# Performance work log

Measured on AMD Instinct MI355X. Metric: run time of the kernel, lower is better.

The kernel has to match this reference:

```python
import jax, jax.numpy as jnp
import numpy as np

B, N, K, H, NHEADS, NIN = 4, 2000, 30, 128, 4, 256
DFF = 4 * H
EPS = 1e-6


def layer_norm(x, gain, bias):
    # torch .var() defaults to unbiased (ddof=1); denominator is (sigma + eps)
    mu = x.mean(-1, keepdims=True)
    sigma = jnp.sqrt(x.var(-1, ddof=1, keepdims=True) + EPS)
    return gain * (x - mu) / (sigma + EPS) + bias


def setup_inputs() -> dict:
    key = jax.random.key(0)
    ks = jax.random.split(key, 10)
    s = 0.05
    h_v = jax.random.normal(ks[0], (B, N, H), jnp.float32)
    h_e = jax.random.normal(ks[1], (B, N, K, NIN), jnp.float32)
    mask_attend = (jax.random.uniform(ks[2], (B, N, K)) < 0.9).astype(jnp.float32)
    mask_attend = mask_attend.at[..., 0].set(1.0)  # avoid all-masked rows -> NaN softmax
    mask_v = (jax.random.uniform(ks[3], (B, N)) < 0.95).astype(jnp.float32)
    return {
        "h_v": h_v,
        "h_e": h_e,
        "mask_v": mask_v,
        "mask_attend": mask_attend,
        "W_Q": jax.random.normal(ks[4], (H, H), jnp.float32) * s,
        "W_K": jax.random.normal(ks[5], (H, NIN), jnp.float32) * s,
        "W_V": jax.random.normal(ks[6], (H, NIN), jnp.float32) * s,
        "W_O": jax.random.normal(ks[7], (H, H), jnp.float32) * s,
        "gain0": jnp.ones((H,), jnp.float32),
        "bias0": jnp.zeros((H,), jnp.float32),
        "gain1": jnp.ones((H,), jnp.float32),
        "bias1": jnp.zeros((H,), jnp.float32),
        "W_in": jax.random.normal(ks[8], (DFF, H), jnp.float32) * s,
        "b_in": jnp.zeros((DFF,), jnp.float32),
        "W_out": jax.random.normal(ks[9], (H, DFF), jnp.float32) * s,
        "b_out": jnp.zeros((H,), jnp.float32),
    }


def reference(h_v, h_e, mask_v, mask_attend, W_Q, W_K, W_V, W_O,
              gain0, bias0, gain1, bias1, W_in, b_in, W_out, b_out):
    d = H // NHEADS
    # Neighbor attention (dropout is identity at inference)
    Q = (h_v @ W_Q.T).reshape(B, N, NHEADS, d)          # [B,N,h,d]
    Kp = (h_e @ W_K.T).reshape(B, N, K, NHEADS, d)      # [B,N,K,h,d]
    Vp = (h_e @ W_V.T).reshape(B, N, K, NHEADS, d)      # [B,N,K,h,d]
    logits = jnp.einsum('bnhd,bnkhd->bnhk', Q, Kp) / np.sqrt(d)
    mask = mask_attend[:, :, None, :]                   # [B,N,1,K] broadcast over heads
    neg_inf = jnp.finfo(logits.dtype).min
    attend = jax.nn.softmax(jnp.where(mask > 0, logits, neg_inf), axis=-1) * mask
    h_upd = jnp.einsum('bnhk,bnkhd->bnhd', attend, Vp).reshape(B, N, H)
    dh = h_upd @ W_O.T
    h = layer_norm(h_v + dh, gain0, bias0)
    # Position-wise FFN
    dh = jax.nn.relu(h @ W_in.T + b_in) @ W_out.T + b_out
    h = layer_norm(h + dh, gain1, bias1)
    return mask_v[..., None] * h
```

## Files before the change

kernel.cpp:

```cpp
#include <hip/hip_runtime.h>
#include <math.h>

#define TK 30
#define TH 128
#define TNIN 256
#define TDFF 512
#define NTOK 8000
#define ROWP 264

typedef __attribute__((ext_vector_type(8))) short short8v;
typedef __attribute__((ext_vector_type(4))) short short4v;
typedef __attribute__((ext_vector_type(4))) float f32x4;

constexpr float LN_EPS = 1e-6f;
constexpr float NEG_INF = -3.402823466e38f;
constexpr float INV_SQRT_D = 0.17677669529663687f;

static __device__ __forceinline__ unsigned short f2bf(float f) {
  unsigned u = __float_as_uint(f);
  u = u + 0x7fffu + ((u >> 16) & 1u);
  return (unsigned short)(u >> 16);
}
static __device__ __forceinline__ float bf2f(unsigned short s) {
  return __uint_as_float(((unsigned)s) << 16);
}
static __device__ __forceinline__ void gload16(const void* gsrc, void* ldst) {
  __builtin_amdgcn_global_load_lds(
      (const __attribute__((address_space(1))) unsigned int*)gsrc,
      (__attribute__((address_space(3))) unsigned int*)ldst, 16, 0, 0);
}

__global__ void conv_weights_kernel(const float* __restrict__ W_K,
                                    const float* __restrict__ W_V,
                                    const float* __restrict__ W_Q,
                                    const float* __restrict__ W_in,
                                    const float* __restrict__ W_out,
                                    unsigned short* __restrict__ Wc2,
                                    unsigned short* __restrict__ Wq2,
                                    unsigned short* __restrict__ Wi2,
                                    unsigned short* __restrict__ Wo2)
{
  int idx = blockIdx.x * 256 + threadIdx.x;
  if (idx < 65536) {
    int e = idx >> 3, j = idx & 7;
    int kk = e >> 10, n = (e >> 6) & 15, lane = e & 63;
    int r = n*16 + (lane & 15);
    int c = kk*32 + (lane >> 4)*8 + j;
    float v = (r < TH) ? W_K[(size_t)r*TNIN + c] : W_V[(size_t)(r-TH)*TNIN + c];
    Wc2[idx] = f2bf(v);
  } else if (idx < 81920) {
    int i2 = idx - 65536;
    int e = i2 >> 3, j = i2 & 7;
    int kk = e >> 9, n = (e >> 6) & 7, lane = e & 63;
    int r = n*16 + (lane & 15);
    int c = kk*32 + (lane >> 4)*8 + j;
    Wq2[i2] = f2bf(W_Q[(size_t)r*TH + c]);
  } else if (idx < 147456) {
    int i3 = idx - 81920;
    int e = i3 >> 3, j = i3 & 7;
    int ks = e >> 11, n = (e >> 6) & 31, lane = e & 63;
    int r = n*16 + (lane & 15);
    int c = ks*32 + (lane >> 4)*8 + j;
    Wi2[i3] = f2bf(W_in[(size_t)r*TH + c]);
  } else {
    int i4 = idx - 147456;
    int e = i4 >> 3, j = i4 & 7;
    int ks = e >> 9, n = (e >> 6) & 7, lane = e & 63;
    int r = n*16 + (lane & 15);
    int c = ks*32 + (lane >> 4)*8 + j;
    Wo2[i4] = f2bf(W_out[(size_t)r*TDFF + c]);
  }
}

__global__ __launch_bounds__(512, 4) void kvattn_kernel(
    const float* __restrict__ A, const unsigned short* __restrict__ Wc2,
    const unsigned short* __restrict__ Qg, const float* __restrict__ mask_attend,
    float* __restrict__ ul)
{
  const int tid  = threadIdx.x;
  const int wave = tid >> 6;
  const int lane = tid & 63;
  const int lm   = lane & 15;
  const int lgp  = lane >> 4;
  const int mh   = wave >> 2;
  const int nq   = wave & 3;

  __shared__ __align__(16) char smem[69632];
  unsigned short* Bl  = (unsigned short*)smem;
  unsigned short* Al  = (unsigned short*)(smem + 49152);
  unsigned short* KVs = (unsigned short*)smem;
  float* att = (float*)(smem + 67584);

  const int rowa = tid >> 2, cga = tid & 3;
  const int rowc = (rowa > 119) ? 119 : rowa;
  const float* aptr = A + ((size_t)blockIdx.x*120 + rowc)*TNIN + cga*8;

  #define ISSUE_B(K)                                                             \
    { gload16(Wc2 + (size_t)(K)*8192 + tid*8,       &Bl[((K)%3)*8192 + tid*8]);  \
      gload16(Wc2 + (size_t)(K)*8192 + (tid+512)*8, &Bl[((K)%3)*8192 + (tid+512)*8]); }

  #define WRITE_A(K, S)                                                     \
    { short8v w;                                                            \
      w[0]=(short)f2bf(ra[S][0].x); w[1]=(short)f2bf(ra[S][0].y);           \
      w[2]=(short)f2bf(ra[S][0].z); w[3]=(short)f2bf(ra[S][0].w);           \
      w[4]=(short)f2bf(ra[S][1].x); w[5]=(short)f2bf(ra[S][1].y);           \
      w[6]=(short)f2bf(ra[S][1].z); w[7]=(short)f2bf(ra[S][1].w);           \
      *(short8v*)&Al[(((K)&1)*128 + rowa)*40 + cga*8] = w; }

  float4 ra[3][2];
  f32x4 acc[4][4] = {};

  ra[0][0] = *(const float4*)(aptr + 0);
  ra[0][1] = *(const float4*)(aptr + 4);
  ISSUE_B(0);
  ISSUE_B(1);
  ra[1][0] = *(const float4*)(aptr + 32);
  ra[1][1] = *(const float4*)(aptr + 36);
  ra[2][0] = *(const float4*)(aptr + 64);
  ra[2][1] = *(const float4*)(aptr + 68);
  WRITE_A(0, 0);

  #pragma unroll
  for (int k = 0; k < 8; ++k) {
    if (k == 7)      asm volatile("s_waitcnt vmcnt(0)" ::: "memory");
    else if (k == 6) asm volatile("s_waitcnt vmcnt(4)" ::: "memory");
    else             asm volatile("s_waitcnt vmcnt(6)" ::: "memory");
    __builtin_amdgcn_s_barrier();

    if (k < 6) ISSUE_B(k+2);
    if (k < 5) {
      ra[k%3][0] = *(const float4*)(aptr + (k+3)*32);
      ra[k%3][1] = *(const float4*)(aptr + (k+3)*32 + 4);
    }

    short8v af[4];
    #pragma unroll
    for (int m = 0; m < 4; ++m)
      af[m] = *(const short8v*)&Al[((k&1)*128 + mh*64 + m*16 + lm)*40 + lgp*8];

    #pragma unroll
    for (int n = 0; n < 4; ++n) {
      short8v b = *(const short8v*)&Bl[(k%3)*8192 + ((nq*4 + n)*64 + lane)*8];
      #pragma unroll
      for (int m = 0; m < 4; ++m)
        acc[m][n] = __builtin_amdgcn_mfma_f32_16x16x32_bf16(b, af[m], acc[m][n], 0, 0, 0);
    }

    if (k < 7) WRITE_A(k+1, (k+1)%3);
  }
  #undef ISSUE_B
  #undef WRITE_A

  __syncthreads();

  #pragma unroll
  for (int m = 0; m < 4; ++m) {
    int row = mh*64 + m*16 + lm;
    #pragma unroll
    for (int n = 0; n < 4; ++n) {
      int col = nq*64 + n*16 + lgp*4;
      short4v p;
      p[0]=(short)f2bf(acc[m][n][0]); p[1]=(short)f2bf(acc[m][n][1]);
      p[2]=(short)f2bf(acc[m][n][2]); p[3]=(short)f2bf(acc[m][n][3]);
      *(short4v*)&KVs[row*ROWP + col] = p;
    }
  }
  __syncthreads();

  {
    int tok = tid >> 7, h = (tid >> 5) & 3, k = tid & 31;
    int gtok = blockIdx.x*4 + tok;
    float s = 0.f;
    float ma = 0.f;
    if (k < TK) {
      const unsigned short* qp = Qg + (size_t)gtok*TH + h*32;
      const unsigned short* kp = &KVs[(tok*TK + k)*ROWP + h*32];
      #pragma unroll
      for (int j = 0; j < 4; ++j) {
        short8v qf = *(const short8v*)(qp + j*8);
        short8v kf = *(const short8v*)(kp + j*8);
        #pragma unroll
        for (int e = 0; e < 8; ++e)
          s += bf2f((unsigned short)qf[e]) * bf2f((unsigned short)kf[e]);
      }
      ma = mask_attend[(size_t)gtok*TK + k];
    }
    bool ok = (k < TK) && (ma > 0.f);
    float val = ok ? s * INV_SQRT_D : NEG_INF;
    float mm = val;
    #pragma unroll
    for (int d = 16; d >= 1; d >>= 1) mm = fmaxf(mm, __shfl_xor(mm, d, 32));
    float e = ok ? expf(val - mm) : 0.f;
    float ss = e;
    #pragma unroll
    for (int d = 16; d >= 1; d >>= 1) ss += __shfl_xor(ss, d, 32);
    att[(tok*4 + h)*32 + k] = e / ss;
  }
  __syncthreads();

  {
    int tok = tid >> 7, c = tid & 127;
    int gtok = blockIdx.x*4 + tok;
    const float* ar = &att[(tok*4 + (c >> 5))*32];
    const unsigned short* vb = &KVs[tok*TK*ROWP + TH + c];
    float u = 0.f;
    #pragma unroll
    for (int k = 0; k < TK; ++k)
      u += ar[k] * bf2f(vb[k*ROWP]);
    ul[(size_t)gtok*TH + c] = u;
  }
}

__global__ __launch_bounds__(512, 4) void q_gemm_kernel(
    const float* __restrict__ h_v, const unsigned short* __restrict__ Wq2,
    unsigned short* __restrict__ Qg)
{
  const int m0   = blockIdx.x * 128;
  const int tid  = threadIdx.x;
  const int wave = tid >> 6;
  const int lane = tid & 63;
  const int lm   = lane & 15;
  const int lgp  = lane >> 4;
  const int mh   = wave >> 2;
  const int nq   = wave & 3;

  __shared__ __align__(16) char smem[53248];
  unsigned short* Bq = (unsigned short*)smem;
  unsigned short* Al = (unsigned short*)(smem + 32768);
  unsigned short* Ct = (unsigned short*)smem;

  const int rowa = tid >> 2, cga = tid & 3;
  int rc = m0 + rowa; if (rc > NTOK-1) rc = NTOK-1;
  const float* aptr = h_v + (size_t)rc*TH + cga*8;

  #define WRITE_A(K, S)                                                     \
    { short8v w;                                                            \
      w[0]=(short)f2bf(ra[S][0].x); w[1]=(short)f2bf(ra[S][0].y);           \
      w[2]=(short)f2bf(ra[S][0].z); w[3]=(short)f2bf(ra[S][0].w);           \
      w[4]=(short)f2bf(ra[S][1].x); w[5]=(short)f2bf(ra[S][1].y);           \
      w[6]=(short)f2bf(ra[S][1].z); w[7]=(short)f2bf(ra[S][1].w);           \
      *(short8v*)&Al[(((K)&1)*128 + rowa)*40 + cga*8] = w; }

  float4 ra[2][2];
  f32x4 acc[4][2] = {};

  ra[0][0] = *(const float4*)(aptr + 0);
  ra[0][1] = *(const float4*)(aptr + 4);
  #pragma unroll
  for (int p = 0; p < 4; ++p)
    gload16(Wq2 + (size_t)(tid + p*512)*8, &Bq[(tid + p*512)*8]);
  ra[1][0] = *(const float4*)(aptr + 32);
  ra[1][1] = *(const float4*)(aptr + 36);
  WRITE_A(0, 0);

  #pragma unroll
  for (int k = 0; k < 4; ++k) {
    if (k == 0) asm volatile("s_waitcnt vmcnt(2)" ::: "memory");
    __builtin_amdgcn_s_barrier();

    if (k < 2) {
      ra[k&1][0] = *(const float4*)(aptr + (k+2)*32);
      ra[k&1][1] = *(const float4*)(aptr + (k+2)*32 + 4);
    }

    short8v af[4];
    #pragma unroll
    for (int m = 0; m < 4; ++m)
      af[m] = *(const short8v*)&Al[((k&1)*128 + mh*64 + m*16 + lm)*40 + lgp*8];

    #pragma unroll
    for (int n = 0; n < 2; ++n) {
      short8v b = *(const short8v*)&Bq[((k*8 + nq*2 + n)*64 + lane)*8];
      #pragma unroll
      for (int m = 0; m < 4; ++m)
        acc[m][n] = __builtin_amdgcn_mfma_f32_16x16x32_bf16(b, af[m], acc[m][n], 0, 0, 0);
    }

    if (k < 3) WRITE_A(k+1, (k+1)&1);
  }
  #undef WRITE_A

  __syncthreads();
  #pragma unroll
  for (int m = 0; m < 4; ++m) {
    int row = mh*64 + m*16 + lm;
    #pragma unroll
    for (int n = 0; n < 2; ++n) {
      int col = nq*32 + n*16 + lgp*4;
      short4v p;
      p[0]=(short)f2bf(acc[m][n][0]); p[1]=(short)f2bf(acc[m][n][1]);
      p[2]=(short)f2bf(acc[m][n][2]); p[3]=(short)f2bf(acc[m][n][3]);
      *(short4v*)&Ct[row*136 + col] = p;
    }
  }
  __syncthreads();
  #pragma unroll
  for (int p = 0; p < 4; ++p) {
    int t = p*512 + tid;
    int row = t >> 4, cg = t & 15;
    if (m0 + row < NTOK)
      *(short8v*)&Qg[(size_t)(m0 + row)*TH + cg*8] =
          *(const short8v*)&Ct[row*136 + cg*8];
  }
}

__global__ __launch_bounds__(256) void wo_ln_kernel(
    const float* __restrict__ ul, const float* __restrict__ W_O,
    const float* __restrict__ h_v, const float* __restrict__ gain0,
    const float* __restrict__ bias0, float* __restrict__ Hn)
{
  const int tid  = threadIdx.x;
  const int tok0 = blockIdx.x * 32;
  __shared__ float Aa[32][128];
  __shared__ float Wt[128][128];

  for (int t = tid; t < 32*32; t += 256) {
    int row = t >> 5, i4 = t & 31;
    *(float4*)&Aa[row][i4*4] = *(const float4*)&ul[(size_t)(tok0+row)*TH + i4*4];
  }
  for (int t = tid; t < 128*32; t += 256) {
    int f = t & 127, i4 = t >> 7;
    float4 w = *(const float4*)&W_O[(size_t)f*TH + i4*4];
    Wt[i4*4+0][f]=w.x; Wt[i4*4+1][f]=w.y; Wt[i4*4+2][f]=w.z; Wt[i4*4+3][f]=w.w;
  }
  __syncthreads();

  const int tokg = tid>>5, colg = tid&31;
  float acc[4][4] = {};
  for (int i = 0; i < TH; i += 4){
    float a[4][4];
    #pragma unroll
    for (int r=0;r<4;r++){
      float4 tv=*(const float4*)&Aa[tokg*4+r][i];
      a[r][0]=tv.x;a[r][1]=tv.y;a[r][2]=tv.z;a[r][3]=tv.w;
    }
    #pragma unroll
    for (int d=0; d<4; ++d){
      float4 wv = *(const float4*)&Wt[i+d][colg*4];
      #pragma unroll
      for (int r=0;r<4;r++){
        acc[r][0]+=a[r][d]*wv.x; acc[r][1]+=a[r][d]*wv.y;
        acc[r][2]+=a[r][d]*wv.z; acc[r][3]+=a[r][d]*wv.w;
      }
    }
  }

  float4 g  = *(const float4*)&gain0[colg*4];
  float4 bb = *(const float4*)&bias0[colg*4];
  #pragma unroll
  for (int r=0;r<4;r++){
    int tok = tok0 + tokg*4 + r;
    float4 hv = *(const float4*)&h_v[(size_t)tok*TH + colg*4];
    float x0 = acc[r][0]+hv.x;
    float x1 = acc[r][1]+hv.y;
    float x2 = acc[r][2]+hv.z;
    float x3 = acc[r][3]+hv.w;
    float s1 = x0+x1+x2+x3;
    float s2 = x0*x0+x1*x1+x2*x2+x3*x3;
    #pragma unroll
    for (int m=16;m>=1;m>>=1){ s1 += __shfl_xor(s1,m,32); s2 += __shfl_xor(s2,m,32); }
    float mu  = s1*(1.f/128.f);
    float var = (s2 - 128.f*mu*mu)*(1.f/127.f);
    float inv = 1.f/(sqrtf(var+LN_EPS)+LN_EPS);
    float4 y;
    y.x = g.x*(x0-mu)*inv + bb.x;
    y.y = g.y*(x1-mu)*inv + bb.y;
    y.z = g.z*(x2-mu)*inv + bb.z;
    y.w = g.w*(x3-mu)*inv + bb.w;
    *(float4*)&Hn[(size_t)tok*TH + colg*4] = y;
  }
}

__global__ __launch_bounds__(256) void ffn_fused_kernel(
    const float* __restrict__ Hn, const unsigned short* __restrict__ Wi2,
    const unsigned short* __restrict__ Wo2,
    const float* __restrict__ b_in, const float* __restrict__ b_out,
    const float* __restrict__ gain1, const float* __restrict__ bias1,
    const float* __restrict__ mask_v, float* __restrict__ out)
{
  const int tid  = threadIdx.x;
  const int tok0 = blockIdx.x * 32;
  const int wave = tid >> 6;
  const int lane = tid & 63;
  const int lm   = lane & 15;
  const int lgp  = lane >> 4;

  __shared__ __align__(16) char bst_mem[32768];
  __shared__ __align__(16) unsigned short At[32][136];
  __shared__ __align__(16) unsigned short Zs[32][520];
  __shared__ float bin[512];
  unsigned short* Bst = (unsigned short*)bst_mem;
  float* Xs = (float*)bst_mem;

  for (int t = tid; t < 1024; t += 256) {
    int row = t >> 5, q = t & 31;
    float4 v = *(const float4*)&Hn[(size_t)(tok0+row)*TH + q*4];
    short4v w;
    w[0]=(short)f2bf(v.x); w[1]=(short)f2bf(v.y);
    w[2]=(short)f2bf(v.z); w[3]=(short)f2bf(v.w);
    *(short4v*)&At[row][q*4] = w;
  }
  if (tid < 128) *(float4*)&bin[tid*4] = *(const float4*)&b_in[tid*4];

  f32x4 acc1[2][8] = {};
  #pragma unroll
  for (int ks = 0; ks < 4; ++ks) {
    #pragma unroll
    for (int p = 0; p < 8; ++p)
      gload16(Wi2 + (size_t)ks*16384 + (tid + p*256)*8, &Bst[(tid + p*256)*8]);
    asm volatile("s_waitcnt vmcnt(0)" ::: "memory");
    __syncthreads();

    short8v a0 = *(const short8v*)&At[lm]     [ks*32 + lgp*8];
    short8v a1 = *(const short8v*)&At[16 + lm][ks*32 + lgp*8];
    #pragma unroll
    for (int n = 0; n < 8; ++n) {
      short8v b = *(const short8v*)&Bst[((wave*8 + n)*64 + lane)*8];
      acc1[0][n] = __builtin_amdgcn_mfma_f32_16x16x32_bf16(b, a0, acc1[0][n], 0, 0, 0);
      acc1[1][n] = __builtin_amdgcn_mfma_f32_16x16x32_bf16(b, a1, acc1[1][n], 0, 0, 0);
    }
    __syncthreads();
  }

  #pragma unroll
  for (int m = 0; m < 2; ++m) {
    int row = m*16 + lm;
    #pragma unroll
    for (int n = 0; n < 8; ++n) {
      int col = (wave*8 + n)*16 + lgp*4;
      float4 bv = *(const float4*)&bin[col];
      short4v p;
      p[0]=(short)f2bf(fmaxf(acc1[m][n][0] + bv.x, 0.f));
      p[1]=(short)f2bf(fmaxf(acc1[m][n][1] + bv.y, 0.f));
      p[2]=(short)f2bf(fmaxf(acc1[m][n][2] + bv.z, 0.f));
      p[3]=(short)f2bf(fmaxf(acc1[m][n][3] + bv.w, 0.f));
      *(short4v*)&Zs[row][col] = p;
    }
  }
  __syncthreads();

  f32x4 acc2[2][2] = {};
  #pragma unroll
  for (int ks2 = 0; ks2 < 8; ++ks2) {
    #pragma unroll
    for (int p = 0; p < 4; ++p)
      gload16(Wo2 + (size_t)ks2*8192 + (tid + p*256)*8, &Bst[(tid + p*256)*8]);
    asm volatile("s_waitcnt vmcnt(0)" ::: "memory");
    __syncthreads();

    #pragma unroll
    for (int s = 0; s < 2; ++s) {
      int ks = ks2*2 + s;
      short8v a0 = *(const short8v*)&Zs[lm]     [ks*32 + lgp*8];
      short8v a1 = *(const short8v*)&Zs[16 + lm][ks*32 + lgp*8];
      #pragma unroll
      for (int n = 0; n < 2; ++n) {
        short8v b = *(const short8v*)&Bst[(s*4096) + ((wave*2 + n)*64 + lane)*8];
        acc2[0][n] = __builtin_amdgcn_mfma_f32_16x16x32_bf16(b, a0, acc2[0][n], 0, 0, 0);
        acc2[1][n] = __builtin_amdgcn_mfma_f32_16x16x32_bf16(b, a1, acc2[1][n], 0, 0, 0);
      }
    }
    __syncthreads();
  }

  #pragma unroll
  for (int m = 0; m < 2; ++m) {
    int row = m*16 + lm;
    #pragma unroll
    for (int n = 0; n < 2; ++n) {
      int col = (wave*2 + n)*16 + lgp*4;
      float4 bo = *(const float4*)&b_out[col];
      float4 hn = *(const float4*)&Hn[(size_t)(tok0+row)*TH + col];
      float4 x;
      x.x = acc2[m][n][0] + bo.x + hn.x;
      x.y = acc2[m][n][1] + bo.y + hn.y;
      x.z = acc2[m][n][2] + bo.z + hn.z;
      x.w = acc2[m][n][3] + bo.w + hn.w;
      *(float4*)&Xs[(size_t)row*132 + col] = x;
    }
  }
  __syncthreads();

  {
    const int tokg = tid >> 5, colg = tid & 31;
    float4 g  = *(const float4*)&gain1[colg*4];
    float4 bb = *(const float4*)&bias1[colg*4];
    float4 bo; (void)bo;
    #pragma unroll
    for (int r = 0; r < 4; ++r) {
      int tok = tok0 + tokg*4 + r;
      float4 xv = *(const float4*)&Xs[(size_t)(tokg*4 + r)*132 + colg*4];
      float x0 = xv.x, x1 = xv.y, x2 = xv.z, x3 = xv.w;
      float s1 = x0+x1+x2+x3;
      float s2 = x0*x0+x1*x1+x2*x2+x3*x3;
      #pragma unroll
      for (int m = 16; m >= 1; m >>= 1) { s1 += __shfl_xor(s1,m,32); s2 += __shfl_xor(s2,m,32); }
      float mu  = s1*(1.f/128.f);
      float var = (s2 - 128.f*mu*mu)*(1.f/127.f);
      float inv = 1.f/(sqrtf(var+LN_EPS)+LN_EPS);
      float mv  = mask_v[tok];
      float4 y;
      y.x = mv*(g.x*(x0-mu)*inv + bb.x);
      y.y = mv*(g.y*(x1-mu)*inv + bb.y);
      y.z = mv*(g.z*(x2-mu)*inv + bb.z);
      y.w = mv*(g.w*(x3-mu)*inv + bb.w);
      *(float4*)&out[(size_t)tok*TH + colg*4] = y;
    }
  }
}

extern "C" void kernel_launch(void* const* d_in, const int* in_sizes, int n_in,
                              void* d_out, int out_size, void* d_ws, size_t ws_size,
                              hipStream_t stream)
{
  const float* h_v         = (const float*)d_in[0];
  const float* h_e         = (const float*)d_in[1];
  const float* mask_v      = (const float*)d_in[2];
  const float* mask_attend = (const float*)d_in[3];
  const float* W_Q   = (const float*)d_in[4];
  const float* W_K   = (const float*)d_in[5];
  const float* W_V   = (const float*)d_in[6];
  const float* W_O   = (const float*)d_in[7];
  const float* gain0 = (const float*)d_in[8];
  const float* bias0 = (const float*)d_in[9];
  const float* gain1 = (const float*)d_in[10];
  const float* bias1 = (const float*)d_in[11];
  const float* W_in  = (const float*)d_in[12];
  const float* b_in  = (const float*)d_in[13];
  const float* W_out = (const float*)d_in[14];
  const float* b_out = (const float*)d_in[15];

  float* out = (float*)d_out;
  char* ws = (char*)d_ws;
  unsigned short* Qg  = (unsigned short*)ws;
  unsigned short* Wc2 = (unsigned short*)(ws + 2048000);
  unsigned short* Wq2 = (unsigned short*)(ws + 2179072);
  unsigned short* Wi2 = (unsigned short*)(ws + 2211840);
  unsigned short* Wo2 = (unsigned short*)(ws + 2342912);
  float* ul = (float*)(ws + 2473984);
  float* Hn = (float*)(ws + 6569984);

  conv_weights_kernel<<<832, 256, 0, stream>>>(W_K, W_V, W_Q, W_in, W_out,
                                               Wc2, Wq2, Wi2, Wo2);
  q_gemm_kernel<<<(NTOK + 127)/128, 512, 0, stream>>>(h_v, Wq2, Qg);
  kvattn_kernel<<<NTOK/4, 512, 0, stream>>>(h_e, Wc2, Qg, mask_attend, ul);
  wo_ln_kernel<<<NTOK/32, 256, 0, stream>>>(ul, W_O, h_v, gain0, bias0, Hn);
  ffn_fused_kernel<<<NTOK/32, 256, 0, stream>>>(Hn, Wi2, Wo2, b_in, b_out,
                                                gain1, bias1, mask_v, out);
}
```

Before: 91.32 us.

## Fuse Q projection into attention and W_O+LN0 into FFN kernel

Removes the separate Q GEMM kernel: each attention block computes Q for its 4 tokens with MFMA from h_v and preloaded W_Q fragments, keeping Q in LDS as fp32. Removes the scalar fp32 W_O+layernorm kernel by converting W_O to bf16 MFMA layout and doing the output projection and first layernorm at the start of the FFN kernel, with Hn kept in registers and LDS. This cuts the launch count from five to three and drops the Qg and Hn round trips through global memory. In exchange the attention kernel uses more LDS and registers, and the W_O product now runs in bf16 instead of fp32.

```diff
diff --git a/kernel.cpp b/kernel.cpp
--- a/kernel.cpp
+++ b/kernel.cpp
@@ -33,10 +33,12 @@
 __global__ void conv_weights_kernel(const float* __restrict__ W_K,
                                     const float* __restrict__ W_V,
                                     const float* __restrict__ W_Q,
+                                    const float* __restrict__ W_O,
                                     const float* __restrict__ W_in,
                                     const float* __restrict__ W_out,
                                     unsigned short* __restrict__ Wc2,
                                     unsigned short* __restrict__ Wq2,
+                                    unsigned short* __restrict__ Wp2,
                                     unsigned short* __restrict__ Wi2,
                                     unsigned short* __restrict__ Wo2)
 {
@@ -55,15 +57,22 @@
     int r = n*16 + (lane & 15);
     int c = kk*32 + (lane >> 4)*8 + j;
     Wq2[i2] = f2bf(W_Q[(size_t)r*TH + c]);
-  } else if (idx < 147456) {
-    int i3 = idx - 81920;
+  } else if (idx < 98304) {
+    int ip = idx - 81920;
+    int e = ip >> 3, j = ip & 7;
+    int kk = e >> 9, n = (e >> 6) & 7, lane = e & 63;
+    int r = n*16 + (lane & 15);
+    int c = kk*32 + (lane >> 4)*8 + j;
+    Wp2[ip] = f2bf(W_O[(size_t)r*TH + c]);
+  } else if (idx < 163840) {
+    int i3 = idx - 98304;
     int e = i3 >> 3, j = i3 & 7;
     int ks = e >> 11, n = (e >> 6) & 31, lane = e & 63;
     int r = n*16 + (lane & 15);
     int c = ks*32 + (lane >> 4)*8 + j;
     Wi2[i3] = f2bf(W_in[(size_t)r*TH + c]);
   } else {
-    int i4 = idx - 147456;
+    int i4 = idx - 163840;
     int e = i4 >> 3, j = i4 & 7;
     int ks = e >> 9, n = (e >> 6) & 7, lane = e & 63;
     int r = n*16 + (lane & 15);
@@ -74,8 +83,8 @@
 
 __global__ __launch_bounds__(512, 4) void kvattn_kernel(
     const float* __restrict__ A, const unsigned short* __restrict__ Wc2,
-    const unsigned short* __restrict__ Qg, const float* __restrict__ mask_attend,
-    float* __restrict__ ul)
+    const unsigned short* __restrict__ Wq2, const float* __restrict__ h_v,
+    const float* __restrict__ mask_attend, float* __restrict__ ul)
 {
   const int tid  = threadIdx.x;
   const int wave = tid >> 6;
@@ -84,12 +93,24 @@
   const int lgp  = lane >> 4;
   const int mh   = wave >> 2;
   const int nq   = wave & 3;
-
-  __shared__ __align__(16) char smem[69632];
+  const int bn0  = blockIdx.x * 4;
+
+  __shared__ __align__(16) char smem[73728];
   unsigned short* Bl  = (unsigned short*)smem;
   unsigned short* Al  = (unsigned short*)(smem + 49152);
   unsigned short* KVs = (unsigned short*)smem;
   float* att = (float*)(smem + 67584);
+  float* hvp = (float*)(smem + 69632);
+  float* qvp = (float*)(smem + 71680);
+
+  short8v wq[4];
+  #pragma unroll
+  for (int ks = 0; ks < 4; ++ks)
+    wq[ks] = *(const short8v*)(Wq2 + ((size_t)(ks*8 + wave)*64 + lane)*8);
+  if (tid < 128) {
+    int tok = tid >> 5, q = tid & 31;
+    *(float4*)&hvp[tok*128 + q*4] = *(const float4*)&h_v[(size_t)(bn0 + tok)*TH + q*4];
+  }
 
   const int rowa = tid >> 2, cga = tid & 3;
   const int rowc = (rowa > 119) ? 119 : rowa;
@@ -151,6 +172,24 @@
   #undef ISSUE_B
   #undef WRITE_A
 
+  {
+    f32x4 qacc = {};
+    const int tokc = (lm < 4) ? lm : 3;
+    #pragma unroll
+    for (int ks = 0; ks < 4; ++ks) {
+      const float* hp = hvp + tokc*128 + ks*32 + lgp*8;
+      float4 lo = *(const float4*)hp;
+      float4 hi = *(const float4*)(hp + 4);
+      short8v ha;
+      ha[0]=(short)f2bf(lo.x); ha[1]=(short)f2bf(lo.y);
+      ha[2]=(short)f2bf(lo.z); ha[3]=(short)f2bf(lo.w);
+      ha[4]=(short)f2bf(hi.x); ha[5]=(short)f2bf(hi.y);
+      ha[6]=(short)f2bf(hi.z); ha[7]=(short)f2bf(hi.w);
+      qacc = __builtin_amdgcn_mfma_f32_16x16x32_bf16(wq[ks], ha, qacc, 0, 0, 0);
+    }
+    if (lm < 4) *(f32x4*)&qvp[lm*128 + wave*16 + lgp*4] = qacc;
+  }
+
   __syncthreads();
 
   #pragma unroll
@@ -169,19 +208,21 @@
 
   {
     int tok = tid >> 7, h = (tid >> 5) & 3, k = tid & 31;
-    int gtok = blockIdx.x*4 + tok;
+    int gtok = bn0 + tok;
     float s = 0.f;
     float ma = 0.f;
     if (k < TK) {
-      const unsigned short* qp = Qg + (size_t)gtok*TH + h*32;
+      const float* qp = &qvp[tok*128 + h*32];
       const unsigned short* kp = &KVs[(tok*TK + k)*ROWP + h*32];
       #pragma unroll
       for (int j = 0; j < 4; ++j) {
-        short8v qf = *(const short8v*)(qp + j*8);
         short8v kf = *(const short8v*)(kp + j*8);
-        #pragma unroll
-        for (int e = 0; e < 8; ++e)
-          s += bf2f((unsigned short)qf[e]) * bf2f((unsigned short)kf[e]);
+        float4 qa = *(const float4*)(qp + j*8);
+        float4 qb = *(const float4*)(qp + j*8 + 4);
+        s += qa.x*bf2f((unsigned short)kf[0]) + qa.y*bf2f((unsigned short)kf[1])
+           + qa.z*bf2f((unsigned short)kf[2]) + qa.w*bf2f((unsigned short)kf[3])
+           + qb.x*bf2f((unsigned short)kf[4]) + qb.y*bf2f((unsigned short)kf[5])
+           + qb.z*bf2f((unsigned short)kf[6]) + qb.w*bf2f((unsigned short)kf[7]);
       }
       ma = mask_attend[(size_t)gtok*TK + k];
     }
@@ -200,7 +241,7 @@
 
   {
     int tok = tid >> 7, c = tid & 127;
-    int gtok = blockIdx.x*4 + tok;
+    int gtok = bn0 + tok;
     const float* ar = &att[(tok*4 + (c >> 5))*32];
     const unsigned short* vb = &KVs[tok*TK*ROWP + TH + c];
     float u = 0.f;
@@ -211,169 +252,11 @@
   }
 }
 
-__global__ __launch_bounds__(512, 4) void q_gemm_kernel(
-    const float* __restrict__ h_v, const unsigned short* __restrict__ Wq2,
-    unsigned short* __restrict__ Qg)
-{
-  const int m0   = blockIdx.x * 128;
-  const int tid  = threadIdx.x;
-  const int wave = tid >> 6;
-  const int lane = tid & 63;
-  const int lm   = lane & 15;
-  const int lgp  = lane >> 4;
-  const int mh   = wave >> 2;
-  const int nq   = wave & 3;
-
-  __shared__ __align__(16) char smem[53248];
-  unsigned short* Bq = (unsigned short*)smem;
-  unsigned short* Al = (unsigned short*)(smem + 32768);
-  unsigned short* Ct = (unsigned short*)smem;
-
-  const int rowa = tid >> 2, cga = tid & 3;
-  int rc = m0 + rowa; if (rc > NTOK-1) rc = NTOK-1;
-  const float* aptr = h_v + (size_t)rc*TH + cga*8;
-
-  #define WRITE_A(K, S)                                                     \
-    { short8v w;                                                            \
-      w[0]=(short)f2bf(ra[S][0].x); w[1]=(short)f2bf(ra[S][0].y);           \
-      w[2]=(short)f2bf(ra[S][0].z); w[3]=(short)f2bf(ra[S][0].w);           \
-      w[4]=(short)f2bf(ra[S][1].x); w[5]=(short)f2bf(ra[S][1].y);           \
-      w[6]=(short)f2bf(ra[S][1].z); w[7]=(short)f2bf(ra[S][1].w);           \
-      *(short8v*)&Al[(((K)&1)*128 + rowa)*40 + cga*8] = w; }
-
-  float4 ra[2][2];
-  f32x4 acc[4][2] = {};
-
-  ra[0][0] = *(const float4*)(aptr + 0);
-  ra[0][1] = *(const float4*)(aptr + 4);
-  #pragma unroll
-  for (int p = 0; p < 4; ++p)
-    gload16(Wq2 + (size_t)(tid + p*512)*8, &Bq[(tid + p*512)*8]);
-  ra[1][0] = *(const float4*)(aptr + 32);
-  ra[1][1] = *(const float4*)(aptr + 36);
-  WRITE_A(0, 0);
-
-  #pragma unroll
-  for (int k = 0; k < 4; ++k) {
-    if (k == 0) asm volatile("s_waitcnt vmcnt(2)" ::: "memory");
-    __builtin_amdgcn_s_barrier();
-
-    if (k < 2) {
-      ra[k&1][0] = *(const float4*)(aptr + (k+2)*32);
-      ra[k&1][1] = *(const float4*)(aptr + (k+2)*32 + 4);
-    }
-
-    short8v af[4];
-    #pragma unroll
-    for (int m = 0; m < 4; ++m)
-      af[m] = *(const short8v*)&Al[((k&1)*128 + mh*64 + m*16 + lm)*40 + lgp*8];
-
-    #pragma unroll
-    for (int n = 0; n < 2; ++n) {
-      short8v b = *(const short8v*)&Bq[((k*8 + nq*2 + n)*64 + lane)*8];
-      #pragma unroll
-      for (int m = 0; m < 4; ++m)
-        acc[m][n] = __builtin_amdgcn_mfma_f32_16x16x32_bf16(b, af[m], acc[m][n], 0, 0, 0);
-    }
-
-    if (k < 3) WRITE_A(k+1, (k+1)&1);
-  }
-  #undef WRITE_A
-
-  __syncthreads();
-  #pragma unroll
-  for (int m = 0; m < 4; ++m) {
-    int row = mh*64 + m*16 + lm;
-    #pragma unroll
-    for (int n = 0; n < 2; ++n) {
-      int col = nq*32 + n*16 + lgp*4;
-      short4v p;
-      p[0]=(short)f2bf(acc[m][n][0]); p[1]=(short)f2bf(acc[m][n][1]);
-      p[2]=(short)f2bf(acc[m][n][2]); p[3]=(short)f2bf(acc[m][n][3]);
-      *(short4v*)&Ct[row*136 + col] = p;
-    }
-  }
-  __syncthreads();
-  #pragma unroll
-  for (int p = 0; p < 4; ++p) {
-    int t = p*512 + tid;
-    int row = t >> 4, cg = t & 15;
-    if (m0 + row < NTOK)
-      *(short8v*)&Qg[(size_t)(m0 + row)*TH + cg*8] =
-          *(const short8v*)&Ct[row*136 + cg*8];
-  }
-}
-
-__global__ __launch_bounds__(256) void wo_ln_kernel(
-    const float* __restrict__ ul, const float* __restrict__ W_O,
-    const float* __restrict__ h_v, const float* __restrict__ gain0,
-    const float* __restrict__ bias0, float* __restrict__ Hn)
-{
-  const int tid  = threadIdx.x;
-  const int tok0 = blockIdx.x * 32;
-  __shared__ float Aa[32][128];
-  __shared__ float Wt[128][128];
-
-  for (int t = tid; t < 32*32; t += 256) {
-    int row = t >> 5, i4 = t & 31;
-    *(float4*)&Aa[row][i4*4] = *(const float4*)&ul[(size_t)(tok0+row)*TH + i4*4];
-  }
-  for (int t = tid; t < 128*32; t += 256) {
-    int f = t & 127, i4 = t >> 7;
-    float4 w = *(const float4*)&W_O[(size_t)f*TH + i4*4];
-    Wt[i4*4+0][f]=w.x; Wt[i4*4+1][f]=w.y; Wt[i4*4+2][f]=w.z; Wt[i4*4+3][f]=w.w;
-  }
-  __syncthreads();
-
-  const int tokg = tid>>5, colg = tid&31;
-  float acc[4][4] = {};
-  for (int i = 0; i < TH; i += 4){
-    float a[4][4];
-    #pragma unroll
-    for (int r=0;r<4;r++){
-      float4 tv=*(const float4*)&Aa[tokg*4+r][i];
-      a[r][0]=tv.x;a[r][1]=tv.y;a[r][2]=tv.z;a[r][3]=tv.w;
-    }
-    #pragma unroll
-    for (int d=0; d<4; ++d){
-      float4 wv = *(const float4*)&Wt[i+d][colg*4];
-      #pragma unroll
-      for (int r=0;r<4;r++){
-        acc[r][0]+=a[r][d]*wv.x; acc[r][1]+=a[r][d]*wv.y;
-        acc[r][2]+=a[r][d]*wv.z; acc[r][3]+=a[r][d]*wv.w;
-      }
-    }
-  }
-
-  float4 g  = *(const float4*)&gain0[colg*4];
-  float4 bb = *(const float4*)&bias0[colg*4];
-  #pragma unroll
-  for (int r=0;r<4;r++){
-    int tok = tok0 + tokg*4 + r;
-    float4 hv = *(const float4*)&h_v[(size_t)tok*TH + colg*4];
-    float x0 = acc[r][0]+hv.x;
-    float x1 = acc[r][1]+hv.y;
-    float x2 = acc[r][2]+hv.z;
-    float x3 = acc[r][3]+hv.w;
-    float s1 = x0+x1+x2+x3;
-    float s2 = x0*x0+x1*x1+x2*x2+x3*x3;
-    #pragma unroll
-    for (int m=16;m>=1;m>>=1){ s1 += __shfl_xor(s1,m,32); s2 += __shfl_xor(s2,m,32); }
-    float mu  = s1*(1.f/128.f);
-    float var = (s2 - 128.f*mu*mu)*(1.f/127.f);
-    float inv = 1.f/(sqrtf(var+LN_EPS)+LN_EPS);
-    float4 y;
-    y.x = g.x*(x0-mu)*inv + bb.x;
-    y.y = g.y*(x1-mu)*inv + bb.y;
-    y.z = g.z*(x2-mu)*inv + bb.z;
-    y.w = g.w*(x3-mu)*inv + bb.w;
-    *(float4*)&Hn[(size_t)tok*TH + colg*4] = y;
-  }
-}
-
-__global__ __launch_bounds__(256) void ffn_fused_kernel(
-    const float* __restrict__ Hn, const unsigned short* __restrict__ Wi2,
-    const unsigned short* __restrict__ Wo2,
+__global__ __launch_bounds__(256, 4) void ffn_all_kernel(
+    const float* __restrict__ ul, const unsigned short* __restrict__ Wp2,
+    const float* __restrict__ h_v,
+    const float* __restrict__ gain0, const float* __restrict__ bias0,
+    const unsigned short* __restrict__ Wi2, const unsigned short* __restrict__ Wo2,
     const float* __restrict__ b_in, const float* __restrict__ b_out,
     const float* __restrict__ gain1, const float* __restrict__ bias1,
     const float* __restrict__ mask_v, float* __restrict__ out)
@@ -385,22 +268,107 @@
   const int lm   = lane & 15;
   const int lgp  = lane >> 4;
 
-  __shared__ __align__(16) char bst_mem[32768];
-  __shared__ __align__(16) unsigned short At[32][136];
-  __shared__ __align__(16) unsigned short Zs[32][520];
-  __shared__ float bin[512];
-  unsigned short* Bst = (unsigned short*)bst_mem;
-  float* Xs = (float*)bst_mem;
+  __shared__ __align__(16) char smem[78336];
+  unsigned short* Bst = (unsigned short*)smem;
+  unsigned short* At  = (unsigned short*)(smem + 32768);
+  unsigned short* Zs  = (unsigned short*)(smem + 41472);
+  float* bin  = (float*)(smem + 74752);
+  float* part = (float*)(smem + 76800);
+  float* red  = (float*)(smem + 77824);
 
   for (int t = tid; t < 1024; t += 256) {
     int row = t >> 5, q = t & 31;
-    float4 v = *(const float4*)&Hn[(size_t)(tok0+row)*TH + q*4];
+    float4 v = *(const float4*)&ul[(size_t)(tok0+row)*TH + q*4];
     short4v w;
     w[0]=(short)f2bf(v.x); w[1]=(short)f2bf(v.y);
     w[2]=(short)f2bf(v.z); w[3]=(short)f2bf(v.w);
-    *(short4v*)&At[row][q*4] = w;
+    *(short4v*)&At[row*136 + q*4] = w;
   }
   if (tid < 128) *(float4*)&bin[tid*4] = *(const float4*)&b_in[tid*4];
+  #pragma unroll
+  for (int p = 0; p < 8; ++p)
+    gload16(Wp2 + (size_t)(tid + p*256)*8, &Bst[(tid + p*256)*8]);
+  asm volatile("s_waitcnt vmcnt(0)" ::: "memory");
+  __syncthreads();
+
+  f32x4 acco[2][2] = {};
+  #pragma unroll
+  for (int ks = 0; ks < 4; ++ks) {
+    short8v a0 = *(const short8v*)&At[lm*136      + ks*32 + lgp*8];
+    short8v a1 = *(const short8v*)&At[(16+lm)*136 + ks*32 + lgp*8];
+    #pragma unroll
+    for (int n = 0; n < 2; ++n) {
+      short8v b = *(const short8v*)&Bst[((size_t)(ks*8 + wave*2 + n)*64 + lane)*8];
+      acco[0][n] = __builtin_amdgcn_mfma_f32_16x16x32_bf16(b, a0, acco[0][n], 0, 0, 0);
+      acco[1][n] = __builtin_amdgcn_mfma_f32_16x16x32_bf16(b, a1, acco[1][n], 0, 0, 0);
+    }
+  }
+
+  f32x4 hn[2][2];
+  {
+    f32x4 x[2][2];
+    float s1r[2] = {0.f, 0.f}, s2r[2] = {0.f, 0.f};
+    #pragma unroll
+    for (int m = 0; m < 2; ++m) {
+      int row = m*16 + lm;
+      #pragma unroll
+      for (int n = 0; n < 2; ++n) {
+        int col = (wave*2 + n)*16 + lgp*4;
+        float4 hv = *(const float4*)&h_v[(size_t)(tok0+row)*TH + col];
+        x[m][n][0] = acco[m][n][0] + hv.x;
+        x[m][n][1] = acco[m][n][1] + hv.y;
+        x[m][n][2] = acco[m][n][2] + hv.z;
+        x[m][n][3] = acco[m][n][3] + hv.w;
+        #pragma unroll
+        for (int r = 0; r < 4; ++r) {
+          s1r[m] += x[m][n][r];
+          s2r[m] += x[m][n][r]*x[m][n][r];
+        }
+      }
+    }
+    #pragma unroll
+    for (int m = 0; m < 2; ++m) {
+      s1r[m] += __shfl_xor(s1r[m], 16); s2r[m] += __shfl_xor(s2r[m], 16);
+      s1r[m] += __shfl_xor(s1r[m], 32); s2r[m] += __shfl_xor(s2r[m], 32);
+    }
+    if (lgp == 0) {
+      part[(lm*4      + wave)*2 + 0] = s1r[0];
+      part[(lm*4      + wave)*2 + 1] = s2r[0];
+      part[((16+lm)*4 + wave)*2 + 0] = s1r[1];
+      part[((16+lm)*4 + wave)*2 + 1] = s2r[1];
+    }
+    __syncthreads();
+    if (tid < 32) {
+      float s1 = 0.f, s2 = 0.f;
+      #pragma unroll
+      for (int w = 0; w < 4; ++w) { s1 += part[(tid*4+w)*2]; s2 += part[(tid*4+w)*2+1]; }
+      float mu  = s1*(1.f/128.f);
+      float var = (s2 - 128.f*mu*mu)*(1.f/127.f);
+      red[tid*2]   = mu;
+      red[tid*2+1] = 1.f/(sqrtf(var+LN_EPS)+LN_EPS);
+    }
+    __syncthreads();
+    #pragma unroll
+    for (int m = 0; m < 2; ++m) {
+      int row = m*16 + lm;
+      float mu = red[row*2], inv = red[row*2+1];
+      #pragma unroll
+      for (int n = 0; n < 2; ++n) {
+        int col = (wave*2 + n)*16 + lgp*4;
+        float4 g = *(const float4*)&gain0[col];
+        float4 b = *(const float4*)&bias0[col];
+        hn[m][n][0] = g.x*(x[m][n][0]-mu)*inv + b.x;
+        hn[m][n][1] = g.y*(x[m][n][1]-mu)*inv + b.y;
+        hn[m][n][2] = g.z*(x[m][n][2]-mu)*inv + b.z;
+        hn[m][n][3] = g.w*(x[m][n][3]-mu)*inv + b.w;
+        short4v p;
+        p[0]=(short)f2bf(hn[m][n][0]); p[1]=(short)f2bf(hn[m][n][1]);
+        p[2]=(short)f2bf(hn[m][n][2]); p[3]=(short)f2bf(hn[m][n][3]);
+        *(short4v*)&At[row*136 + col] = p;
+      }
+    }
+  }
+  __syncthreads();
 
   f32x4 acc1[2][8] = {};
   #pragma unroll
@@ -411,8 +379,8 @@
     asm volatile("s_waitcnt vmcnt(0)" ::: "memory");
     __syncthreads();
 
-    short8v a0 = *(const short8v*)&At[lm]     [ks*32 + lgp*8];
-    short8v a1 = *(const short8v*)&At[16 + lm][ks*32 + lgp*8];
+    short8v a0 = *(const short8v*)&At[lm*136      + ks*32 + lgp*8];
+    short8v a1 = *(const short8v*)&At[(16+lm)*136 + ks*32 + lgp*8];
     #pragma unroll
     for (int n = 0; n < 8; ++n) {
       short8v b = *(const short8v*)&Bst[((wave*8 + n)*64 + lane)*8];
@@ -434,7 +402,7 @@
       p[1]=(short)f2bf(fmaxf(acc1[m][n][1] + bv.y, 0.f));
       p[2]=(short)f2bf(fmaxf(acc1[m][n][2] + bv.z, 0.f));
       p[3]=(short)f2bf(fmaxf(acc1[m][n][3] + bv.w, 0.f));
-      *(short4v*)&Zs[row][col] = p;
+      *(short4v*)&Zs[row*520 + col] = p;
     }
   }
   __syncthreads();
@@ -451,8 +419,8 @@
     #pragma unroll
     for (int s = 0; s < 2; ++s) {
       int ks = ks2*2 + s;
-      short8v a0 = *(const short8v*)&Zs[lm]     [ks*32 + lgp*8];
-      short8v a1 = *(const short8v*)&Zs[16 + lm][ks*32 + lgp*8];
+      short8v a0 = *(const short8v*)&Zs[lm*520      + ks*32 + lgp*8];
+      short8v a1 = *(const short8v*)&Zs[(16+lm)*520 + ks*32 + lgp*8];
       #pragma unroll
       for (int n = 0; n < 2; ++n) {
         short8v b = *(const short8v*)&Bst[(s*4096) + ((wave*2 + n)*64 + lane)*8];
@@ -463,48 +431,65 @@
     __syncthreads();
   }
 
-  #pragma unroll
-  for (int m = 0; m < 2; ++m) {
-    int row = m*16 + lm;
-    #pragma unroll
-    for (int n = 0; n < 2; ++n) {
-      int col = (wave*2 + n)*16 + lgp*4;
-      float4 bo = *(const float4*)&b_out[col];
-      float4 hn = *(const float4*)&Hn[(size_t)(tok0+row)*TH + col];
-      float4 x;
-      x.x = acc2[m][n][0] + bo.x + hn.x;
-      x.y = acc2[m][n][1] + bo.y + hn.y;
-      x.z = acc2[m][n][2] + bo.z + hn.z;
-      x.w = acc2[m][n][3] + bo.w + hn.w;
-      *(float4*)&Xs[(size_t)row*132 + col] = x;
-    }
-  }
-  __syncthreads();
-
   {
-    const int tokg = tid >> 5, colg = tid & 31;
-    float4 g  = *(const float4*)&gain1[colg*4];
-    float4 bb = *(const float4*)&bias1[colg*4];
-    float4 bo; (void)bo;
-    #pragma unroll
-    for (int r = 0; r < 4; ++r) {
-      int tok = tok0 + tokg*4 + r;
-      float4 xv = *(const float4*)&Xs[(size_t)(tokg*4 + r)*132 + colg*4];
-      float x0 = xv.x, x1 = xv.y, x2 = xv.z, x3 = xv.w;
-      float s1 = x0+x1+x2+x3;
-      float s2 = x0*x0+x1*x1+x2*x2+x3*x3;
-      #pragma unroll
-      for (int m = 16; m >= 1; m >>= 1) { s1 += __shfl_xor(s1,m,32); s2 += __shfl_xor(s2,m,32); }
+    f32x4 x[2][2];
+    float s1r[2] = {0.f, 0.f}, s2r[2] = {0.f, 0.f};
+    #pragma unroll
+    for (int m = 0; m < 2; ++m) {
+      #pragma unroll
+      for (int n = 0; n < 2; ++n) {
+        int col = (wave*2 + n)*16 + lgp*4;
+        float4 bo = *(const float4*)&b_out[col];
+        x[m][n][0] = acc2[m][n][0] + bo.x + hn[m][n][0];
+        x[m][n][1] = acc2[m][n][1] + bo.y + hn[m][n][1];
+        x[m][n][2] = acc2[m][n][2] + bo.z + hn[m][n][2];
+        x[m][n][3] = acc2[m][n][3] + bo.w + hn[m][n][3];
+        #pragma unroll
+        for (int r = 0; r < 4; ++r) {
+          s1r[m] += x[m][n][r];
+          s2r[m] += x[m][n][r]*x[m][n][r];
+        }
+      }
+    }
+    #pragma unroll
+    for (int m = 0; m < 2; ++m) {
+      s1r[m] += __shfl_xor(s1r[m], 16); s2r[m] += __shfl_xor(s2r[m], 16);
+      s1r[m] += __shfl_xor(s1r[m], 32); s2r[m] += __shfl_xor(s2r[m], 32);
+    }
+    if (lgp == 0) {
+      part[(lm*4      + wave)*2 + 0] = s1r[0];
+      part[(lm*4      + wave)*2 + 1] = s2r[0];
+      part[((16+lm)*4 + wave)*2 + 0] = s1r[1];
+      part[((16+lm)*4 + wave)*2 + 1] = s2r[1];
+    }
+    __syncthreads();
+    if (tid < 32) {
+      float s1 = 0.f, s2 = 0.f;
+      #pragma unroll
+      for (int w = 0; w < 4; ++w) { s1 += part[(tid*4+w)*2]; s2 += part[(tid*4+w)*2+1]; }
       float mu  = s1*(1.f/128.f);
       float var = (s2 - 128.f*mu*mu)*(1.f/127.f);
-      float inv = 1.f/(sqrtf(var+LN_EPS)+LN_EPS);
-      float mv  = mask_v[tok];
-      float4 y;
-      y.x = mv*(g.x*(x0-mu)*inv + bb.x);
-      y.y = mv*(g.y*(x1-mu)*inv + bb.y);
-      y.z = mv*(g.z*(x2-mu)*inv + bb.z);
-      y.w = mv*(g.w*(x3-mu)*inv + bb.w);
-      *(float4*)&out[(size_t)tok*TH + colg*4] = y;
+      red[tid*2]   = mu;
+      red[tid*2+1] = 1.f/(sqrtf(var+LN_EPS)+LN_EPS);
+    }
+    __syncthreads();
+    #pragma unroll
+    for (int m = 0; m < 2; ++m) {
+      int row = m*16 + lm;
+      float mu = red[row*2], inv = red[row*2+1];
+      float mv = mask_v[tok0 + row];
+      #pragma unroll
+      for (int n = 0; n < 2; ++n) {
+        int col = (wave*2 + n)*16 + lgp*4;
+        float4 g = *(const float4*)&gain1[col];
+        float4 b = *(const float4*)&bias1[col];
+        float4 y;
+        y.x = mv*(g.x*(x[m][n][0]-mu)*inv + b.x);
+        y.y = mv*(g.y*(x[m][n][1]-mu)*inv + b.y);
+        y.z = mv*(g.z*(x[m][n][2]-mu)*inv + b.z);
+        y.w = mv*(g.w*(x[m][n][3]-mu)*inv + b.w);
+        *(float4*)&out[(size_t)(tok0+row)*TH + col] = y;
+      }
     }
   }
 }
@@ -532,19 +517,17 @@
 
   float* out = (float*)d_out;
   char* ws = (char*)d_ws;
-  unsigned short* Qg  = (unsigned short*)ws;
-  unsigned short* Wc2 = (unsigned short*)(ws + 2048000);
-  unsigned short* Wq2 = (unsigned short*)(ws + 2179072);
-  unsigned short* Wi2 = (unsigned short*)(ws + 2211840);
-  unsigned short* Wo2 = (unsigned short*)(ws + 2342912);
-  float* ul = (float*)(ws + 2473984);
-  float* Hn = (float*)(ws + 6569984);
-
-  conv_weights_kernel<<<832, 256, 0, stream>>>(W_K, W_V, W_Q, W_in, W_out,
-                                               Wc2, Wq2, Wi2, Wo2);
-  q_gemm_kernel<<<(NTOK + 127)/128, 512, 0, stream>>>(h_v, Wq2, Qg);
-  kvattn_kernel<<<NTOK/4, 512, 0, stream>>>(h_e, Wc2, Qg, mask_attend, ul);
-  wo_ln_kernel<<<NTOK/32, 256, 0, stream>>>(ul, W_O, h_v, gain0, bias0, Hn);
-  ffn_fused_kernel<<<NTOK/32, 256, 0, stream>>>(Hn, Wi2, Wo2, b_in, b_out,
-                                                gain1, bias1, mask_v, out);
-}
+  unsigned short* Wc2 = (unsigned short*)ws;
+  unsigned short* Wq2 = (unsigned short*)(ws + 131072);
+  unsigned short* Wp2 = (unsigned short*)(ws + 163840);
+  unsigned short* Wi2 = (unsigned short*)(ws + 196608);
+  unsigned short* Wo2 = (unsigned short*)(ws + 327680);
+  float* ul = (float*)(ws + 458752);
+
+  conv_weights_kernel<<<896, 256, 0, stream>>>(W_K, W_V, W_Q, W_O, W_in, W_out,
+                                               Wc2, Wq2, Wp2, Wi2, Wo2);
+  kvattn_kernel<<<NTOK/4, 512, 0, stream>>>(h_e, Wc2, Wq2, h_v, mask_attend, ul);
+  ffn_all_kernel<<<NTOK/32, 256, 0, stream>>>(ul, Wp2, h_v, gain0, bias0,
+                                              Wi2, Wo2, b_in, b_out,
+                                              gain1, bias1, mask_v, out);
+}
```

Result: slower. 104.4 us (+14.3%).
